# Kernel tuning notes

Measured on AMD Instinct MI355X. Metric: run time of the kernel, lower is better.

## Reference

```python
import jax, jax.numpy as jnp
import numpy as np

NEG_SLOPE = 0.2


def gatv2_layer(x, edge_index, Wl, Wr, att, bias):
    """PyG GATv2Conv (share_weights=False, concat=True, negative_slope=0.2).
    x: [N, F]; Wl/Wr: [F, H*C]; att: [H, C]; bias: [H*C]. Returns [N, H*C]."""
    N = x.shape[0]
    H, C = att.shape
    src, dst = edge_index[0], edge_index[1]
    xl = (x @ Wl).reshape(N, H, C)  # source transform
    xr = (x @ Wr).reshape(N, H, C)  # target transform
    # per-edge attention logits
    e = jax.nn.leaky_relu(xl[src] + xr[dst], NEG_SLOPE)          # [E, H, C]
    logits = jnp.einsum('ehc,hc->eh', e, att)                     # [E, H]
    # segment softmax over incoming edges of each destination node
    m = jax.ops.segment_max(logits, dst, num_segments=N)          # [N, H]
    m = jnp.where(jnp.isfinite(m), m, 0.0)                        # empty segments
    ex = jnp.exp(logits - m[dst])                                 # [E, H]
    denom = jax.ops.segment_sum(ex, dst, num_segments=N)          # [N, H]
    alpha = ex / (denom[dst] + 1e-16)                             # [E, H]
    msg = xl[src] * alpha[..., None]                              # [E, H, C]
    out = jax.ops.segment_sum(msg, dst, num_segments=N)           # [N, H, C]
    return out.reshape(N, H * C) + bias


def setup_inputs() -> dict:
    key = jax.random.key(0)
    ks = jax.random.split(key, 10)
    N, E, F, H, C, OUT = 50000, 800000, 256, 8, 32, 64
    s = 0.05
    return {
        'x': jax.random.normal(ks[0], (N, F), dtype=jnp.float32),
        'edge_index': jax.random.randint(ks[1], (2, E), 0, N, dtype=jnp.int64),
        'Wl1': jax.random.normal(ks[2], (F, H * C), dtype=jnp.float32) * s,
        'Wr1': jax.random.normal(ks[3], (F, H * C), dtype=jnp.float32) * s,
        'att1': jax.random.normal(ks[4], (H, C), dtype=jnp.float32) * s,
        'b1': jax.random.normal(ks[5], (H * C,), dtype=jnp.float32) * s,
        'Wl2': jax.random.normal(ks[6], (H * C, OUT), dtype=jnp.float32) * s,
        'Wr2': jax.random.normal(ks[7], (H * C, OUT), dtype=jnp.float32) * s,
        'att2': jax.random.normal(ks[8], (1, OUT), dtype=jnp.float32) * s,
        'b2': jax.random.normal(ks[9], (OUT,), dtype=jnp.float32) * s,
    }


def reference(x, edge_index, Wl1, Wr1, att1, b1, Wl2, Wr2, att2, b2):
    h = gatv2_layer(x, edge_index, Wl1, Wr1, att1, b1)
    h = jax.nn.relu(h)
    h = gatv2_layer(h, edge_index, Wl2, Wr2, att2, b2)
    return (h, jax.nn.log_softmax(h, axis=1))
```

## Files before the change

### kernel.cpp

```cpp
#include <hip/hip_runtime.h>
#include <hip/hip_bf16.h>
#include <math.h>

#define NEG_SLOPE 0.2f

typedef __attribute__((ext_vector_type(8))) short short8;
typedef __attribute__((ext_vector_type(4))) float floatx4;
typedef __attribute__((ext_vector_type(2))) float floatx2;

__device__ inline ushort f2b(float f) {
    __hip_bfloat16 b = __float2bfloat16(f);
    return *(ushort*)&b;
}
__device__ inline floatx2 bf2x2(unsigned int d) {
    union { unsigned int i; float f; } lo, hi;
    lo.i = d << 16;
    hi.i = d & 0xffff0000u;
    floatx2 r = {lo.f, hi.f};
    return r;
}

template<int BM, int BN, int KTOT>
__global__ __launch_bounds__(256) void gemm_bf16(const ushort* __restrict__ A,
                                                 const ushort* __restrict__ Bt,
                                                 ushort* __restrict__ C,
                                                 int M, int N)
{
    constexpr int SA = 40;
    constexpr int WTM = (BN == 64) ? 32 : 64;
    constexpr int WM  = BM / WTM;
    constexpr int IT  = WTM / 16;
    constexpr int JT  = 4;
    __shared__ ushort As[BM * SA];
    __shared__ ushort Bs[BN * SA];
    const int tid = threadIdx.x;
    const int w = tid >> 6, lane = tid & 63;
    const int mw = (w % WM) * WTM;
    const int nw = (w / WM) * 64;
    const int m0 = blockIdx.y * BM;
    const int n0 = blockIdx.x * BN;
    const int lm = lane & 15;
    const int kg = lane >> 4;

    const int srow = tid >> 2, skc = tid & 3;

    const ushort* aSrc[BM / 64];
#pragma unroll
    for (int it = 0; it < BM / 64; ++it) {
        int grow = m0 + it * 64 + srow;
        if (grow >= M) grow = M - 1;
        aSrc[it] = A + (size_t)grow * KTOT + skc * 8;
    }
    const ushort* bSrc[BN / 64];
#pragma unroll
    for (int it = 0; it < BN / 64; ++it)
        bSrc[it] = Bt + (size_t)(n0 + it * 64 + srow) * KTOT + skc * 8;

    floatx4 acc[IT][JT];
#pragma unroll
    for (int i = 0; i < IT; ++i)
#pragma unroll
        for (int j = 0; j < JT; ++j) acc[i][j] = (floatx4)0.f;

#pragma unroll
    for (int k0 = 0; k0 < KTOT; k0 += 32) {
#pragma unroll
        for (int it = 0; it < BM / 64; ++it) {
            short8 v = *(const short8*)(aSrc[it] + k0);
            *(short8*)&As[(it * 64 + srow) * SA + skc * 8] = v;
        }
#pragma unroll
        for (int it = 0; it < BN / 64; ++it) {
            short8 v = *(const short8*)(bSrc[it] + k0);
            *(short8*)&Bs[(it * 64 + srow) * SA + skc * 8] = v;
        }
        __syncthreads();
        short8 a[IT], b[JT];
#pragma unroll
        for (int i = 0; i < IT; ++i)
            a[i] = *(const short8*)&As[(mw + i * 16 + lm) * SA + kg * 8];
#pragma unroll
        for (int j = 0; j < JT; ++j)
            b[j] = *(const short8*)&Bs[(nw + j * 16 + lm) * SA + kg * 8];
#pragma unroll
        for (int i = 0; i < IT; ++i)
#pragma unroll
            for (int j = 0; j < JT; ++j)
                acc[i][j] = __builtin_amdgcn_mfma_f32_16x16x32_bf16(a[i], b[j], acc[i][j], 0, 0, 0);
        __syncthreads();
    }

#pragma unroll
    for (int i = 0; i < IT; ++i) {
        int rbase = m0 + mw + i * 16 + (lane >> 4) * 4;
#pragma unroll
        for (int j = 0; j < JT; ++j) {
            int col = n0 + nw + j * 16 + lm;
#pragma unroll
            for (int r = 0; r < 4; ++r) {
                int row = rbase + r;
                if (row < M) C[(size_t)row * N + col] = f2b(acc[i][j][r]);
            }
        }
    }
}

__global__ void k_prep(const float* __restrict__ x, ushort* __restrict__ xb, int XB,
                       const float* __restrict__ Wl1, const float* __restrict__ Wr1,
                       const float* __restrict__ Wl2, const float* __restrict__ Wr2,
                       ushort* __restrict__ wlr1t, ushort* __restrict__ wlr2t,
                       const int* __restrict__ dst, int E, int* __restrict__ counts16)
{
    const int b = blockIdx.x;
    const int t = threadIdx.x;
    if (b < XB) {
        int i = b * 2048 + t * 8;
        float4 f0 = *(const float4*)&x[i];
        float4 f1 = *(const float4*)&x[i + 4];
        short8 o;
        o[0] = (short)f2b(f0.x); o[1] = (short)f2b(f0.y);
        o[2] = (short)f2b(f0.z); o[3] = (short)f2b(f0.w);
        o[4] = (short)f2b(f1.x); o[5] = (short)f2b(f1.y);
        o[6] = (short)f2b(f1.z); o[7] = (short)f2b(f1.w);
        *(short8*)&xb[i] = o;
    } else if (b < XB + 640) {
        int i = (b - XB) * 256 + t;
        if (i < 65536) {
            int k = i >> 8, n = i & 255;
            wlr1t[n * 256 + k] = f2b(Wl1[i]);
        } else if (i < 131072) {
            int j = i - 65536;
            int k = j >> 8, n = j & 255;
            wlr1t[65536 + n * 256 + k] = f2b(Wr1[j]);
        } else if (i < 147456) {
            int j = i - 131072;
            int k = j >> 6, n = j & 63;
            wlr2t[n * 256 + k] = f2b(Wl2[j]);
        } else {
            int j = i - 147456;
            int k = j >> 6, n = j & 63;
            wlr2t[16384 + n * 256 + k] = f2b(Wr2[j]);
        }
    } else {
        int i = (b - XB - 640) * 256 + t;
        if (i < E) atomicAdd(&counts16[dst[i] * 16], 1);
    }
}

__global__ void k_chunksum(const int* __restrict__ counts16, int N, int* __restrict__ chunk)
{
    __shared__ int sm[256];
    const int t = threadIdx.x;
    const int base = blockIdx.x * 1024;
    int s = 0;
    for (int i = t; i < 1024; i += 256) {
        int idx = base + i;
        s += (idx < N) ? counts16[idx * 16] : 0;
    }
    sm[t] = s;
    __syncthreads();
    for (int off = 128; off; off >>= 1) {
        if (t < off) sm[t] += sm[t + off];
        __syncthreads();
    }
    if (t == 0) chunk[blockIdx.x] = sm[0];
}

__global__ void k_scanfinish(const int* __restrict__ counts16, int N,
                             const int* __restrict__ chunk, int nchunks,
                             int* __restrict__ offsets, int* __restrict__ cursor16)
{
    __shared__ int sm[256];
    __shared__ int s_pref, s_total;
    const int t = threadIdx.x;
    if (t < 64) {
        int v = (t < nchunks) ? chunk[t] : 0;
        int inc = v;
#pragma unroll
        for (int off = 1; off < 64; off <<= 1) {
            int y = __shfl_up(inc, off);
            if (t >= off) inc += y;
        }
        if (t == (int)blockIdx.x) s_pref = inc - v;
        if (t == 63) s_total = inc;
    }
    __syncthreads();
    const int base = blockIdx.x * 1024 + t * 4;
    int v[4];
    int s = 0;
#pragma unroll
    for (int i = 0; i < 4; ++i) {
        v[i] = (base + i < N) ? counts16[(base + i) * 16] : 0;
        s += v[i];
    }
    sm[t] = s;
    __syncthreads();
    for (int off = 1; off < 256; off <<= 1) {
        int y = (t >= off) ? sm[t - off] : 0;
        __syncthreads();
        sm[t] += y;
        __syncthreads();
    }
    int run = s_pref + sm[t] - s;
#pragma unroll
    for (int i = 0; i < 4; ++i) {
        if (base + i < N) {
            offsets[base + i] = run;
            cursor16[(base + i) * 16] = run;
        }
        run += v[i];
    }
    if (blockIdx.x == 0 && t == 0) offsets[N] = s_total;
}

__global__ void k_fill(const int* __restrict__ src, const int* __restrict__ dst,
                       int E, int* __restrict__ cursor16, int* __restrict__ csr_off)
{
    int i = blockIdx.x * blockDim.x + threadIdx.x;
    if (i < E) {
        int d = dst[i];
        int pos = atomicAdd(&cursor16[d * 16], 1);
        csr_off[pos] = src[i] * 1024;
    }
    if (i < 16) csr_off[E + i] = 0;
}

__global__ __launch_bounds__(256) void agg1(const ushort* __restrict__ xlr,
                                            const float* __restrict__ att,
                                            const float* __restrict__ bias,
                                            const int* __restrict__ offsets,
                                            const int* __restrict__ csr_off,
                                            ushort* __restrict__ h1, int N)
{
    const int wave = blockIdx.x * 4 + (threadIdx.x >> 6);
    const int lane = threadIdx.x & 63;
    if (wave >= N) return;
    const int n = wave;
    const int g = lane >> 5;
    const int sl = lane & 31;
    const int elem = (sl >> 2) * 32 + (sl & 3) * 8;
    const char* __restrict__ xbase = (const char*)xlr;
    const int ebyte = elem * 2;

    floatx2 attv2[4], xrv2[4];
    {
        uint4 xr8 = *(const uint4*)(xbase + (size_t)n * 1024 + 512 + ebyte);
        unsigned int xw[4] = {xr8.x, xr8.y, xr8.z, xr8.w};
#pragma unroll
        for (int i = 0; i < 4; ++i) {
            attv2[i] = *(const floatx2*)&att[elem + 2 * i];
            xrv2[i] = bf2x2(xw[i]);
        }
    }
    float m = -1e30f, l = 0.f;
    floatx2 acc2[4] = {(floatx2)0.f, (floatx2)0.f, (floatx2)0.f, (floatx2)0.f};

    const int beg = offsets[n], end = offsets[n + 1];
    uint4 vA, vB;
    int oC;
    {
        int k0 = beg + g;
        vA = *(const uint4*)(xbase + (unsigned)csr_off[k0] + ebyte);
        vB = *(const uint4*)(xbase + (unsigned)csr_off[k0 + 2] + ebyte);
        oC = csr_off[k0 + 4];
    }
    for (int kk = beg + g; kk < end; kk += 2) {
        uint4 cur = vA;
        vA = vB;
        vB = *(const uint4*)(xbase + (unsigned)oC + ebyte);
        oC = csr_off[kk + 6];

        unsigned int cw[4] = {cur.x, cur.y, cur.z, cur.w};
        floatx2 xl2[4];
        floatx2 u2 = (floatx2)0.f;
#pragma unroll
        for (int i = 0; i < 4; ++i) {
            xl2[i] = bf2x2(cw[i]);
            floatx2 t = xl2[i] + xrv2[i];
            t = __builtin_elementwise_max(t, t * NEG_SLOPE);
            u2 += t * attv2[i];
        }
        float u = u2.x + u2.y;
        u += __shfl_xor(u, 1);
        u += __shfl_xor(u, 2);
        float e = __expf(-fabsf(u - m));
        bool kp = (m >= u);
        float sc = kp ? 1.f : e;
        float p  = kp ? e : 1.f;
        m = fmaxf(m, u);
#pragma unroll
        for (int i = 0; i < 4; ++i) acc2[i] = acc2[i] * sc + xl2[i] * p;
        l = fmaf(l, sc, p);
    }
    {
        float mo = __shfl_xor(m, 32);
        float lo = __shfl_xor(l, 32);
        float nm = fmaxf(m, mo);
        float ea = __expf(m - nm);
        float eb = __expf(mo - nm);
#pragma unroll
        for (int i = 0; i < 4; ++i) {
            floatx2 ao = {__shfl_xor(acc2[i].x, 32), __shfl_xor(acc2[i].y, 32)};
            acc2[i] = acc2[i] * ea + ao * eb;
        }
        l = l * ea + lo * eb;
    }
    if (g == 0) {
        float rl = 1.f / (l + 1e-16f);
        short8 o;
#pragma unroll
        for (int i = 0; i < 4; ++i) {
            float v0 = fmaf(acc2[i].x, rl, bias[elem + 2 * i]);
            float v1 = fmaf(acc2[i].y, rl, bias[elem + 2 * i + 1]);
            o[2 * i]     = (short)f2b(fmaxf(v0, 0.f));
            o[2 * i + 1] = (short)f2b(fmaxf(v1, 0.f));
        }
        *(short8*)&h1[(size_t)n * 256 + elem] = o;
    }
}

__global__ __launch_bounds__(256) void agg2(const ushort* __restrict__ xlr,
                                            const float* __restrict__ att,
                                            const float* __restrict__ bias,
                                            const int* __restrict__ offsets,
                                            const int* __restrict__ csr_off,
                                            float* __restrict__ out, int N)
{
    const int wave = blockIdx.x * 4 + (threadIdx.x >> 6);
    const int lane = threadIdx.x & 63;
    const int n = wave * 2 + (lane >> 5);
    if (n >= N) return;
    const int sub = lane & 31;
    const int g = sub >> 3;
    const int cl = sub & 7;
    const char* __restrict__ xbase = (const char*)xlr;
    const int cbyte = cl * 16;

    floatx2 attv2[4], xrv2[4];
    {
        uint4 xr8 = *(const uint4*)(xbase + (size_t)n * 256 + 128 + cbyte);
        unsigned int xw[4] = {xr8.x, xr8.y, xr8.z, xr8.w};
#pragma unroll
        for (int i = 0; i < 4; ++i) {
            attv2[i] = *(const floatx2*)&att[cl * 8 + 2 * i];
            xrv2[i] = bf2x2(xw[i]);
        }
    }
    float m = -1e30f, l = 0.f;
    floatx2 acc2[4] = {(floatx2)0.f, (floatx2)0.f, (floatx2)0.f, (floatx2)0.f};

    const int beg = offsets[n], end = offsets[n + 1];
    uint4 vA;
    int oB;
    {
        int k0 = beg + g;
        vA = *(const uint4*)(xbase + ((unsigned)csr_off[k0] >> 2) + cbyte);
        oB = csr_off[k0 + 4];
    }
    for (int kk = beg + g; kk < end; kk += 4) {
        uint4 cur = vA;
        vA = *(const uint4*)(xbase + ((unsigned)oB >> 2) + cbyte);
        oB = csr_off[kk + 8];

        unsigned int cw[4] = {cur.x, cur.y, cur.z, cur.w};
        floatx2 xl2[4];
        floatx2 u2 = (floatx2)0.f;
#pragma unroll
        for (int i = 0; i < 4; ++i) {
            xl2[i] = bf2x2(cw[i]);
            floatx2 t = xl2[i] + xrv2[i];
            t = __builtin_elementwise_max(t, t * NEG_SLOPE);
            u2 += t * attv2[i];
        }
        float u = u2.x + u2.y;
        u += __shfl_xor(u, 1);
        u += __shfl_xor(u, 2);
        u += __shfl_xor(u, 4);
        float e = __expf(-fabsf(u - m));
        bool kp = (m >= u);
        float sc = kp ? 1.f : e;
        float p  = kp ? e : 1.f;
        m = fmaxf(m, u);
#pragma unroll
        for (int i = 0; i < 4; ++i) acc2[i] = acc2[i] * sc + xl2[i] * p;
        l = fmaf(l, sc, p);
    }
#pragma unroll
    for (int off = 8; off <= 16; off <<= 1) {
        float mo = __shfl_xor(m, off);
        float lo = __shfl_xor(l, off);
        float nm = fmaxf(m, mo);
        float sa = __expf(m - nm);
        float sb = __expf(mo - nm);
#pragma unroll
        for (int i = 0; i < 4; ++i) {
            floatx2 ao = {__shfl_xor(acc2[i].x, off), __shfl_xor(acc2[i].y, off)};
            acc2[i] = acc2[i] * sa + ao * sb;
        }
        l = l * sa + lo * sb;
        m = nm;
    }
    float rl = 1.f / (l + 1e-16f);
    float h[8];
#pragma unroll
    for (int i = 0; i < 4; ++i) {
        h[2 * i]     = fmaf(acc2[i].x, rl, bias[cl * 8 + 2 * i]);
        h[2 * i + 1] = fmaf(acc2[i].y, rl, bias[cl * 8 + 2 * i + 1]);
    }

    float mx = h[0];
#pragma unroll
    for (int i = 1; i < 8; ++i) mx = fmaxf(mx, h[i]);
    mx = fmaxf(mx, __shfl_xor(mx, 1));
    mx = fmaxf(mx, __shfl_xor(mx, 2));
    mx = fmaxf(mx, __shfl_xor(mx, 4));
    float ssum = 0.f;
#pragma unroll
    for (int i = 0; i < 8; ++i) ssum += __expf(h[i] - mx);
    ssum += __shfl_xor(ssum, 1);
    ssum += __shfl_xor(ssum, 2);
    ssum += __shfl_xor(ssum, 4);
    float lg = mx + __logf(ssum);
    if (g == 0) {
        float4 o0 = make_float4(h[0], h[1], h[2], h[3]);
        float4 o1 = make_float4(h[4], h[5], h[6], h[7]);
        *(float4*)&out[(size_t)n * 64 + cl * 8] = o0;
        *(float4*)&out[(size_t)n * 64 + cl * 8 + 4] = o1;
        float4 s0 = make_float4(h[0] - lg, h[1] - lg, h[2] - lg, h[3] - lg);
        float4 s1 = make_float4(h[4] - lg, h[5] - lg, h[6] - lg, h[7] - lg);
        *(float4*)&out[(size_t)(N + n) * 64 + cl * 8] = s0;
        *(float4*)&out[(size_t)(N + n) * 64 + cl * 8 + 4] = s1;
    }
}

extern "C" void kernel_launch(void* const* d_in, const int* in_sizes, int n_in,
                              void* d_out, int out_size, void* d_ws, size_t ws_size,
                              hipStream_t stream)
{
    const float* x    = (const float*)d_in[0];
    const int*   ei   = (const int*)d_in[1];
    const float* Wl1  = (const float*)d_in[2];
    const float* Wr1  = (const float*)d_in[3];
    const float* att1 = (const float*)d_in[4];
    const float* b1   = (const float*)d_in[5];
    const float* Wl2  = (const float*)d_in[6];
    const float* Wr2  = (const float*)d_in[7];
    const float* att2 = (const float*)d_in[8];
    const float* b2   = (const float*)d_in[9];
    float* out = (float*)d_out;

    const int F = 256;
    const int E = in_sizes[1] / 2;
    const int N = in_sizes[0] / F;

    const int* e_src = ei;
    const int* e_dst = ei + E;

    ushort* xb    = (ushort*)d_ws;
    ushort* wlr1t = xb + (size_t)N * 256;
    ushort* wlr2t = wlr1t + 512 * 256;
    ushort* xlr1  = wlr2t + 128 * 256;
    ushort* h1b   = xlr1 + (size_t)N * 512;
    ushort* xlr2  = h1b + (size_t)N * 256;
    int* offsets  = (int*)(xlr2 + (size_t)N * 128);
    int* chunkoff = offsets + (N + 1);
    int* csr_off  = chunkoff + 66;
    int* counts16 = csr_off + E + 16;
    int* cursor16 = counts16 + (size_t)N * 16;

    const int nchunks = (N + 1023) / 1024;
    const int XB = (N * 256) / 2048;

    hipMemsetAsync(counts16, 0, (size_t)N * 16 * sizeof(int), stream);
    k_prep<<<XB + 640 + (E + 255) / 256, 256, 0, stream>>>(
        x, xb, XB, Wl1, Wr1, Wl2, Wr2, wlr1t, wlr2t, e_dst, E, counts16);

    gemm_bf16<128, 128, 256><<<dim3(4, (N + 127) / 128), 256, 0, stream>>>(xb, wlr1t, xlr1, N, 512);

    k_chunksum<<<nchunks, 256, 0, stream>>>(counts16, N, chunkoff);
    k_scanfinish<<<nchunks, 256, 0, stream>>>(counts16, N, chunkoff, nchunks, offsets, cursor16);
    k_fill<<<(E + 255) / 256, 256, 0, stream>>>(e_src, e_dst, E, cursor16, csr_off);

    agg1<<<(N + 3) / 4, 256, 0, stream>>>(xlr1, att1, b1, offsets, csr_off, h1b, N);

    gemm_bf16<128, 64, 256><<<dim3(2, (N + 127) / 128), 256, 0, stream>>>(h1b, wlr2t, xlr2, N, 128);
    agg2<<<(N + 7) / 8, 256, 0, stream>>>(xlr2, att2, b2, offsets, csr_off, out, N);
}
```

Before: 330.1 us.

## Fuse CSR construction into one persistent kernel with grid barriers

Replaces the memset, the degree-count section of k_prep, and the chunk-sum, scan and fill kernels with a single 256-block persistent kernel. Its stages are separated by atomic-counter grid barriers, and it zeroes the counts itself. The goal is to remove several kernel launches and their inter-kernel gaps. In exchange the atomic and fill phases run on only 256 blocks, and the spin barriers assume all blocks are co-resident. The chunk scan also assumes N/256 ≤ 256 nodes per block.

```diff
diff --git a/kernel.cpp b/kernel.cpp
--- a/kernel.cpp
+++ b/kernel.cpp
@@ -3,6 +3,7 @@
 #include <math.h>
 
 #define NEG_SLOPE 0.2f
+#define CSRG 256
 
 typedef __attribute__((ext_vector_type(8))) short short8;
 typedef __attribute__((ext_vector_type(4))) float floatx4;
@@ -41,7 +42,6 @@
     const int n0 = blockIdx.x * BN;
     const int lm = lane & 15;
     const int kg = lane >> 4;
-
     const int srow = tid >> 2, skc = tid & 3;
 
     const ushort* aSrc[BM / 64];
@@ -108,8 +108,7 @@
 __global__ void k_prep(const float* __restrict__ x, ushort* __restrict__ xb, int XB,
                        const float* __restrict__ Wl1, const float* __restrict__ Wr1,
                        const float* __restrict__ Wl2, const float* __restrict__ Wr2,
-                       ushort* __restrict__ wlr1t, ushort* __restrict__ wlr2t,
-                       const int* __restrict__ dst, int E, int* __restrict__ counts16)
+                       ushort* __restrict__ wlr1t, ushort* __restrict__ wlr2t)
 {
     const int b = blockIdx.x;
     const int t = threadIdx.x;
@@ -123,7 +122,7 @@
         o[4] = (short)f2b(f1.x); o[5] = (short)f2b(f1.y);
         o[6] = (short)f2b(f1.z); o[7] = (short)f2b(f1.w);
         *(short8*)&xb[i] = o;
-    } else if (b < XB + 640) {
+    } else {
         int i = (b - XB) * 256 + t;
         if (i < 65536) {
             int k = i >> 8, n = i & 255;
@@ -141,59 +140,63 @@
             int k = j >> 6, n = j & 63;
             wlr2t[16384 + n * 256 + k] = f2b(Wr2[j]);
         }
-    } else {
-        int i = (b - XB - 640) * 256 + t;
-        if (i < E) atomicAdd(&counts16[dst[i] * 16], 1);
-    }
-}
-
-__global__ void k_chunksum(const int* __restrict__ counts16, int N, int* __restrict__ chunk)
-{
+    }
+}
+
+__device__ __forceinline__ void gbar(int* ctr, int target)
+{
+    __syncthreads();
+    if (threadIdx.x == 0) {
+        __threadfence();
+        __hip_atomic_fetch_add(ctr, 1, __ATOMIC_ACQ_REL, __HIP_MEMORY_SCOPE_AGENT);
+        while (__hip_atomic_load(ctr, __ATOMIC_ACQUIRE, __HIP_MEMORY_SCOPE_AGENT) < target)
+            __builtin_amdgcn_s_sleep(2);
+    }
+    __syncthreads();
+}
+
+__global__ __launch_bounds__(256) void k_csr(const int* __restrict__ src,
+                                             const int* __restrict__ dst,
+                                             int E, int N,
+                                             int* __restrict__ counts16,
+                                             int* __restrict__ cursor16,
+                                             int* __restrict__ offsets,
+                                             int* __restrict__ chunksum,
+                                             int* __restrict__ bar,
+                                             int* __restrict__ csr_off)
+{
+    const int t = threadIdx.x, b = blockIdx.x;
+    const int gtid = b * 256 + t;
+    const int GT = CSRG * 256;
     __shared__ int sm[256];
-    const int t = threadIdx.x;
-    const int base = blockIdx.x * 1024;
-    int s = 0;
-    for (int i = t; i < 1024; i += 256) {
-        int idx = base + i;
-        s += (idx < N) ? counts16[idx * 16] : 0;
-    }
-    sm[t] = s;
+
+    {
+        int4* p = (int4*)counts16;
+        const int tot4 = N * 4;
+        int4 z = make_int4(0, 0, 0, 0);
+        for (int i = gtid; i < tot4; i += GT) p[i] = z;
+    }
+    gbar(&bar[0], CSRG);
+
+    for (int i = gtid; i < E; i += GT)
+        __hip_atomic_fetch_add(&counts16[dst[i] * 16], 1,
+                               __ATOMIC_RELAXED, __HIP_MEMORY_SCOPE_AGENT);
+    gbar(&bar[1], CSRG);
+
+    const int CH = (N + CSRG - 1) / CSRG;
+    const int n = b * CH + t;
+    int v = (t < CH && n < N) ? counts16[n * 16] : 0;
+    sm[t] = v;
     __syncthreads();
     for (int off = 128; off; off >>= 1) {
         if (t < off) sm[t] += sm[t + off];
         __syncthreads();
     }
-    if (t == 0) chunk[blockIdx.x] = sm[0];
-}
-
-__global__ void k_scanfinish(const int* __restrict__ counts16, int N,
-                             const int* __restrict__ chunk, int nchunks,
-                             int* __restrict__ offsets, int* __restrict__ cursor16)
-{
-    __shared__ int sm[256];
-    __shared__ int s_pref, s_total;
-    const int t = threadIdx.x;
-    if (t < 64) {
-        int v = (t < nchunks) ? chunk[t] : 0;
-        int inc = v;
-#pragma unroll
-        for (int off = 1; off < 64; off <<= 1) {
-            int y = __shfl_up(inc, off);
-            if (t >= off) inc += y;
-        }
-        if (t == (int)blockIdx.x) s_pref = inc - v;
-        if (t == 63) s_total = inc;
-    }
-    __syncthreads();
-    const int base = blockIdx.x * 1024 + t * 4;
-    int v[4];
-    int s = 0;
-#pragma unroll
-    for (int i = 0; i < 4; ++i) {
-        v[i] = (base + i < N) ? counts16[(base + i) * 16] : 0;
-        s += v[i];
-    }
-    sm[t] = s;
+    if (t == 0) chunksum[b] = sm[0];
+    gbar(&bar[2], CSRG);
+
+    int cv = chunksum[t];
+    sm[t] = cv;
     __syncthreads();
     for (int off = 1; off < 256; off <<= 1) {
         int y = (t >= off) ? sm[t - off] : 0;
@@ -201,28 +204,32 @@
         sm[t] += y;
         __syncthreads();
     }
-    int run = s_pref + sm[t] - s;
-#pragma unroll
-    for (int i = 0; i < 4; ++i) {
-        if (base + i < N) {
-            offsets[base + i] = run;
-            cursor16[(base + i) * 16] = run;
-        }
-        run += v[i];
-    }
-    if (blockIdx.x == 0 && t == 0) offsets[N] = s_total;
-}
-
-__global__ void k_fill(const int* __restrict__ src, const int* __restrict__ dst,
-                       int E, int* __restrict__ cursor16, int* __restrict__ csr_off)
-{
-    int i = blockIdx.x * blockDim.x + threadIdx.x;
-    if (i < E) {
+    const int total = sm[255];
+    const int base = (b == 0) ? 0 : sm[b - 1];
+    __syncthreads();
+    sm[t] = v;
+    __syncthreads();
+    for (int off = 1; off < 256; off <<= 1) {
+        int y = (t >= off) ? sm[t - off] : 0;
+        __syncthreads();
+        sm[t] += y;
+        __syncthreads();
+    }
+    int excl = base + sm[t] - v;
+    if (t < CH && n < N) {
+        offsets[n] = excl;
+        cursor16[n * 16] = excl;
+    }
+    if (b == CSRG - 1 && t == 0) offsets[N] = total;
+    gbar(&bar[3], CSRG);
+
+    for (int i = gtid; i < E; i += GT) {
         int d = dst[i];
-        int pos = atomicAdd(&cursor16[d * 16], 1);
+        int pos = __hip_atomic_fetch_add(&cursor16[d * 16], 1,
+                                         __ATOMIC_RELAXED, __HIP_MEMORY_SCOPE_AGENT);
         csr_off[pos] = src[i] * 1024;
     }
-    if (i < 16) csr_off[E + i] = 0;
+    if (gtid < 16) csr_off[E + gtid] = 0;
 }
 
 __global__ __launch_bounds__(256) void agg1(const ushort* __restrict__ xlr,
@@ -463,23 +470,22 @@
     ushort* h1b   = xlr1 + (size_t)N * 512;
     ushort* xlr2  = h1b + (size_t)N * 256;
     int* offsets  = (int*)(xlr2 + (size_t)N * 128);
-    int* chunkoff = offsets + (N + 1);
-    int* csr_off  = chunkoff + 66;
+    int* chunksum = offsets + (N + 1);
+    int* bar      = chunksum + 256;
+    int* csr_off  = bar + 16;
     int* counts16 = csr_off + E + 16;
     int* cursor16 = counts16 + (size_t)N * 16;
 
-    const int nchunks = (N + 1023) / 1024;
     const int XB = (N * 256) / 2048;
 
-    hipMemsetAsync(counts16, 0, (size_t)N * 16 * sizeof(int), stream);
-    k_prep<<<XB + 640 + (E + 255) / 256, 256, 0, stream>>>(
-        x, xb, XB, Wl1, Wr1, Wl2, Wr2, wlr1t, wlr2t, e_dst, E, counts16);
+    hipMemsetAsync(bar, 0, 4 * sizeof(int), stream);
+
+    k_prep<<<XB + 640, 256, 0, stream>>>(x, xb, XB, Wl1, Wr1, Wl2, Wr2, wlr1t, wlr2t);
 
     gemm_bf16<128, 128, 256><<<dim3(4, (N + 127) / 128), 256, 0, stream>>>(xb, wlr1t, xlr1, N, 512);
 
-    k_chunksum<<<nchunks, 256, 0, stream>>>(counts16, N, chunkoff);
-    k_scanfinish<<<nchunks, 256, 0, stream>>>(counts16, N, chunkoff, nchunks, offsets, cursor16);
-    k_fill<<<(E + 255) / 256, 256, 0, stream>>>(e_src, e_dst, E, cursor16, csr_off);
+    k_csr<<<CSRG, 256, 0, stream>>>(e_src, e_dst, E, N, counts16, cursor16,
+                                    offsets, chunksum, bar, csr_off);
 
     agg1<<<(N + 3) / 4, 256, 0, stream>>>(xlr1, att1, b1, offsets, csr_off, h1b, N);
 
```

Result: slower. 415.9 us (+26.0%).
